# Kernel tuning notes

Hardware: AMD Instinct MI355X
Metric: run time of the kernel (lower is better)

## Reference

```python
import jax, jax.numpy as jnp
import numpy as np

B, C, L, E = 65536, 16, 32, 32
EPS = 1e-12

def _normalize(x, axis=-1):
    # F.normalize: x / max(||x||_2, eps)
    n = jnp.sqrt(jnp.sum(x * x, axis=axis, keepdims=True))
    return x / jnp.maximum(n, EPS)

def _linear(x, W, b):
    # torch nn.Linear: y = x @ W.T + b, W: [out, in]
    return jnp.einsum('bcl,el->bce', x, W) + b

def setup_inputs() -> dict:
    key = jax.random.key(0)
    ks = jax.random.split(key, 12)
    s_l = 1.0 / np.sqrt(L)
    s_p1 = 1.0 / np.sqrt(C * E)
    s_p2 = 1.0 / np.sqrt(C * 3)
    return {
        'embed1': jax.random.normal(ks[0], (B, C, L), jnp.float32),
        'embed2': jax.random.normal(ks[1], (B, C, L), jnp.float32),
        'qW': jax.random.uniform(ks[2], (E, L), jnp.float32, -s_l, s_l),
        'qb': jax.random.uniform(ks[3], (E,), jnp.float32, -s_l, s_l),
        'kW': jax.random.uniform(ks[4], (E, L), jnp.float32, -s_l, s_l),
        'kb': jax.random.uniform(ks[5], (E,), jnp.float32, -s_l, s_l),
        'vW': jax.random.uniform(ks[6], (E, L), jnp.float32, -s_l, s_l),
        'vb': jax.random.uniform(ks[7], (E,), jnp.float32, -s_l, s_l),
        'p1W': jax.random.uniform(ks[8], (C * 3, C * E), jnp.float32, -s_p1, s_p1),
        'p1b': jax.random.uniform(ks[9], (C * 3,), jnp.float32, -s_p1, s_p1),
        'p2W': jax.random.uniform(ks[10], (3, C * 3), jnp.float32, -s_p2, s_p2),
        'p2b': jax.random.uniform(ks[11], (3,), jnp.float32, -s_p2, s_p2),
    }

def reference(embed1, embed2, qW, qb, kW, kb, vW, vb, p1W, p1b, p2W, p2b):
    query = _linear(embed1, qW, qb) * _linear(embed2, qW, qb)   # [B,C,E]
    key_t = _linear(embed1, kW, kb) * _linear(embed2, kW, kb)   # [B,C,E]
    value = _linear(embed1, vW, vb) * _linear(embed2, vW, vb)   # [B,C,E]
    attn = jnp.einsum('bce,bde->bcd', _normalize(query), _normalize(key_t))  # [B,C,C]
    # torch F.softmax with dim=None on a 3-D tensor -> legacy dim=0 (batch axis)
    attn = jax.nn.softmax(attn, axis=0)
    # dropout(p=0.2) is identity in eval mode
    out = jnp.einsum('bcd,bce->bde', attn, value)  # attn.transpose(1,2) @ value, [B,C,E]
    h = out.reshape(out.shape[0], -1)              # [B, C*E]
    h = jax.nn.relu(h @ p1W.T + p1b) @ p2W.T + p2b  # [B, 3]
    return _normalize(h)
```

## Files before the change

### kernel.cpp

```cpp
#include <hip/hip_runtime.h>

#define B_TOT 65536
#define WS_P1W 4096
#define WS_EV  (1u << 20)

typedef float f32x4 __attribute__((ext_vector_type(4)));
typedef short s16x8 __attribute__((ext_vector_type(8)));

__device__ __forceinline__ float bf2f(unsigned short h) {
    unsigned u = ((unsigned)h) << 16;
    return __builtin_bit_cast(float, u);
}
__device__ __forceinline__ unsigned pack2(float a, float b) {
    unsigned ua = __builtin_bit_cast(unsigned, a) + 0x8000u;
    unsigned ub = __builtin_bit_cast(unsigned, b) + 0x8000u;
    return __builtin_amdgcn_perm(ub, ua, 0x07060302u);
}
__device__ __forceinline__ unsigned short f2bf(float f) {
    return (unsigned short)((__builtin_bit_cast(unsigned, f) + 0x8000u) >> 16);
}
__device__ __forceinline__ s16x8 cvt8(float4 a, float4 b) {
    uint4 u;
    u.x = pack2(a.x, a.y); u.y = pack2(a.z, a.w);
    u.z = pack2(b.x, b.y); u.w = pack2(b.z, b.w);
    return __builtin_bit_cast(s16x8, u);
}
#define MFMA(a, b, c) __builtin_amdgcn_mfma_f32_16x16x32_bf16((a), (b), (c), 0, 0, 0)

__global__ __launch_bounds__(256) void k0_prep(const float* __restrict__ p1W,
                                               char* __restrict__ ws) {
    int idx = blockIdx.x * 256 + threadIdx.x;
    if (blockIdx.x == 0 && threadIdx.x < 256)
        ((float*)ws)[threadIdx.x] = 0.f;
    int jj   = idx & 7;
    int lane = (idx >> 3) & 63;
    int ktnt = idx >> 9;
    int kt = ktnt & 15, nt = ktnt >> 4;
    int n_lo = lane & 15, q8 = lane >> 4;
    int j  = nt * 16 + n_lo;
    int ip = kt * 32 + q8 * 8 + jj;
    int e_lo = ip >> 5, qq = (ip >> 3) & 3, hh = (ip >> 2) & 1, r = ip & 3;
    int orig = (qq * 4 + r) * 32 + (e_lo + 16 * hh);
    ((unsigned short*)(ws + WS_P1W))[idx] = f2bf(p1W[j * 512 + orig]);
}

__global__ __launch_bounds__(256) void k1_stats(
    const float* __restrict__ e1, const float* __restrict__ e2,
    const float* __restrict__ qW, const float* __restrict__ qb,
    const float* __restrict__ kW, const float* __restrict__ kb,
    const float* __restrict__ vW, const float* __restrict__ vb,
    char* __restrict__ ws) {

    const int tid = threadIdx.x;
    const int lane = tid & 63;
    const int widx = tid >> 6;
    const int col = lane & 15;
    const int quad = lane >> 4;

    __shared__ __align__(16) unsigned short qk_lds[4][2][16 * 40];
    __shared__ float Dblk[256];
    Dblk[tid] = 0.f;
    __syncthreads();

    s16x8 wq[2], wk[2], wv[2];
    f32x4 cbq[2], cbk[2], cbv[2];
    for (int h = 0; h < 2; ++h) {
        int row = col + 16 * h;
        const float4* pq = (const float4*)(qW + row * 32 + quad * 8);
        const float4* pk = (const float4*)(kW + row * 32 + quad * 8);
        const float4* pv = (const float4*)(vW + row * 32 + quad * 8);
        wq[h] = cvt8(pq[0], pq[1]);
        wk[h] = cvt8(pk[0], pk[1]);
        wv[h] = cvt8(pv[0], pv[1]);
        float qv = qb[row], kv = kb[row], vv = vb[row];
        cbq[h] = (f32x4){qv, qv, qv, qv};
        cbk[h] = (f32x4){kv, kv, kv, kv};
        cbv[h] = (f32x4){vv, vv, vv, vv};
    }

    unsigned short* qbuf = qk_lds[widx][0];
    unsigned short* kbuf = qk_lds[widx][1];
    float dacc[4] = {0.f, 0.f, 0.f, 0.f};
    char* evbase = ws + WS_EV;
    const f32x4 z = {0.f, 0.f, 0.f, 0.f};

    const int gw = blockIdx.x * 4 + widx;
    for (int i = 0; i < 8; ++i) {
        const int b = gw * 8 + i;
        const float4* x1p = (const float4*)(e1 + (size_t)b * 512 + col * 32 + quad * 8);
        const float4* x2p = (const float4*)(e2 + (size_t)b * 512 + col * 32 + quad * 8);
        float4 a0 = x1p[0], a1 = x1p[1];
        float4 b0 = x2p[0], b1 = x2p[1];
        s16x8 fx1 = cvt8(a0, a1);
        s16x8 fx2 = cvt8(b0, b1);

        f32x4 q1[2], q2[2], k1[2], k2[2], v1[2], v2[2];
        for (int h = 0; h < 2; ++h) {
            q1[h] = MFMA(fx1, wq[h], cbq[h]); q2[h] = MFMA(fx2, wq[h], cbq[h]);
            k1[h] = MFMA(fx1, wk[h], cbk[h]); k2[h] = MFMA(fx2, wk[h], cbk[h]);
            v1[h] = MFMA(fx1, wv[h], cbv[h]); v2[h] = MFMA(fx2, wv[h], cbv[h]);
        }
        float Qt[2][4], Kt[2][4], Vv[2][4];
        for (int h = 0; h < 2; ++h)
            for (int r = 0; r < 4; ++r) {
                Qt[h][r] = q1[h][r] * q2[h][r];
                Kt[h][r] = k1[h][r] * k2[h][r];
                Vv[h][r] = v1[h][r] * v2[h][r];
            }
        for (int r = 0; r < 4; ++r) {
            int w = (quad * 4 + r) * 20 + col;
            ((unsigned*)qbuf)[w] = pack2(Qt[0][r], Qt[1][r]);
            ((unsigned*)kbuf)[w] = pack2(Kt[0][r], Kt[1][r]);
        }
        s16x8 aq = *(const s16x8*)(qbuf + col * 40 + quad * 8);
        s16x8 bk = *(const s16x8*)(kbuf + col * 40 + quad * 8);
        float qv[8], kv[8], ssq = 0.f, ssk = 0.f;
        for (int j = 0; j < 8; ++j) {
            qv[j] = bf2f((unsigned short)aq[j]); ssq += qv[j] * qv[j];
            kv[j] = bf2f((unsigned short)bk[j]); ssk += kv[j] * kv[j];
        }
        ssq += __shfl_xor(ssq, 16); ssq += __shfl_xor(ssq, 32);
        ssk += __shfl_xor(ssk, 16); ssk += __shfl_xor(ssk, 32);
        float sq = 1.f / fmaxf(sqrtf(ssq), 1e-12f);
        float sk = 1.f / fmaxf(sqrtf(ssk), 1e-12f);
        uint4 uq, uk;
        uq.x = pack2(qv[0] * sq, qv[1] * sq); uq.y = pack2(qv[2] * sq, qv[3] * sq);
        uq.z = pack2(qv[4] * sq, qv[5] * sq); uq.w = pack2(qv[6] * sq, qv[7] * sq);
        uk.x = pack2(kv[0] * sk, kv[1] * sk); uk.y = pack2(kv[2] * sk, kv[3] * sk);
        uk.z = pack2(kv[4] * sk, kv[5] * sk); uk.w = pack2(kv[6] * sk, kv[7] * sk);
        aq = __builtin_bit_cast(s16x8, uq);
        bk = __builtin_bit_cast(s16x8, uk);
        f32x4 S = MFMA(aq, bk, z);

        char* bbase = evbase + (size_t)b * 1536;
        float ex[4];
        for (int r = 0; r < 4; ++r) { ex[r] = __expf(S[r]); dacc[r] += ex[r]; }
        uint2 est; est.x = pack2(ex[0], ex[1]); est.y = pack2(ex[2], ex[3]);
        *(uint2*)(bbase + col * 32 + quad * 8) = est;
        for (int h = 0; h < 2; ++h) {
            uint2 vst;
            vst.x = pack2(Vv[h][0], Vv[h][1]);
            vst.y = pack2(Vv[h][2], Vv[h][3]);
            *(uint2*)(bbase + 512 + ((h * 16 + col) * 2 + (quad >> 1)) * 16 + (quad & 1) * 8) = vst;
        }
    }
    for (int r = 0; r < 4; ++r)
        atomicAdd(&Dblk[col * 16 + quad * 4 + r], dacc[r]);
    __syncthreads();
    atomicAdd(((float*)ws) + tid, Dblk[tid]);
}

__global__ __launch_bounds__(256) void k2_apply(
    const char* __restrict__ ws, const float* __restrict__ p1b,
    const float* __restrict__ p2W, const float* __restrict__ p2b,
    float* __restrict__ out) {

    const int tid = threadIdx.x;
    const int lane = tid & 63;
    const int widx = tid >> 6;
    const int col = lane & 15;
    const int quad = lane >> 4;
    const int qm = quad & 1;

    __shared__ __align__(16) unsigned short Hs[16 * 512];
    float* P = (float*)Hs;

    const float* Dws = (const float*)ws;
    float dinv[8];
    for (int j = 0; j < 8; ++j)
        dinv[j] = 1.f / Dws[col * 16 + qm * 8 + j];

    const char* evbase = ws + WS_EV;
    const unsigned short* p1wp = (const unsigned short*)(ws + WS_P1W);
    const int g = blockIdx.x;
    const f32x4 z = {0.f, 0.f, 0.f, 0.f};
    const s16x8 zz = {0, 0, 0, 0, 0, 0, 0, 0};

    for (int ii = 0; ii < 4; ++ii) {
        const int i = widx * 4 + ii;
        const int b = g * 16 + i;
        const char* bbase = evbase + (size_t)b * 1536;
        s16x8 eraw = *(const s16x8*)(bbase + col * 32 + qm * 16);
        s16x8 bf0 = *(const s16x8*)(bbase + 512 + (col * 2 + qm) * 16);
        s16x8 bf1 = *(const s16x8*)(bbase + 512 + ((16 + col) * 2 + qm) * 16);
        float ef[8];
        for (int j = 0; j < 8; ++j)
            ef[j] = bf2f((unsigned short)eraw[j]) * dinv[j];
        uint4 ua;
        ua.x = pack2(ef[0], ef[1]); ua.y = pack2(ef[2], ef[3]);
        ua.z = pack2(ef[4], ef[5]); ua.w = pack2(ef[6], ef[7]);
        s16x8 afrag = __builtin_bit_cast(s16x8, ua);
        if (quad >= 2) { afrag = zz; bf0 = zz; bf1 = zz; }
        f32x4 o0 = MFMA(afrag, bf0, z);
        f32x4 o1 = MFMA(afrag, bf1, z);
        uint4 uh;
        uh.x = pack2(o0[0], o0[1]); uh.y = pack2(o0[2], o0[3]);
        uh.z = pack2(o1[0], o1[1]); uh.w = pack2(o1[2], o1[3]);
        int chunk = (col * 4 + quad) ^ (i & 7);
        *(uint4*)(Hs + i * 512 + chunk * 8) = uh;
    }
    __syncthreads();

    f32x4 acc[3] = {z, z, z};
    for (int t = 0; t < 4; ++t) {
        int kt = widx * 4 + t;
        int chunk = (kt * 4 + quad) ^ (col & 7);
        s16x8 a = *(const s16x8*)(Hs + col * 512 + chunk * 8);
        for (int nt = 0; nt < 3; ++nt) {
            s16x8 bw = *(const s16x8*)(p1wp + ((nt * 16 + kt) * 64 + lane) * 8);
            acc[nt] = MFMA(a, bw, acc[nt]);
        }
    }
    __syncthreads();

    for (int nt = 0; nt < 3; ++nt)
        *(f32x4*)(P + (widx * 64 + lane) * 12 + nt * 4) = acc[nt];
    __syncthreads();

    if (widx == 0) {
        f32x4 s[3] = {z, z, z};
        for (int w = 0; w < 4; ++w)
            for (int nt = 0; nt < 3; ++nt) {
                f32x4 pv = *(const f32x4*)(P + (w * 64 + lane) * 12 + nt * 4);
                s[nt] += pv;
            }
        float p2w[3][3], p1bias[3];
        for (int nt = 0; nt < 3; ++nt) {
            p1bias[nt] = p1b[col + 16 * nt];
            for (int t = 0; t < 3; ++t) p2w[nt][t] = p2W[t * 48 + col + 16 * nt];
        }
        const float pb0 = p2b[0], pb1 = p2b[1], pb2 = p2b[2];
        float pp[4][3] = {};
        for (int nt = 0; nt < 3; ++nt)
            for (int r = 0; r < 4; ++r) {
                float hv = fmaxf(s[nt][r] + p1bias[nt], 0.f);
                pp[r][0] += hv * p2w[nt][0];
                pp[r][1] += hv * p2w[nt][1];
                pp[r][2] += hv * p2w[nt][2];
            }
        for (int m = 1; m <= 8; m <<= 1)
            for (int r = 0; r < 4; ++r)
                for (int t = 0; t < 3; ++t)
                    pp[r][t] += __shfl_xor(pp[r][t], m);
        for (int r = 0; r < 4; ++r) {
            float h0 = pp[r][0] + pb0, h1 = pp[r][1] + pb1, h2 = pp[r][2] + pb2;
            float inv = 1.f / fmaxf(sqrtf(h0 * h0 + h1 * h1 + h2 * h2), 1e-12f);
            if (col < 3) {
                float v = (col == 0) ? h0 : ((col == 1) ? h1 : h2);
                out[(size_t)(g * 16 + quad * 4 + r) * 3 + col] = v * inv;
            }
        }
    }
}

extern "C" void kernel_launch(void* const* d_in, const int* in_sizes, int n_in,
                              void* d_out, int out_size, void* d_ws, size_t ws_size,
                              hipStream_t stream) {
    const float* e1  = (const float*)d_in[0];
    const float* e2  = (const float*)d_in[1];
    const float* qW  = (const float*)d_in[2];
    const float* qb  = (const float*)d_in[3];
    const float* kW  = (const float*)d_in[4];
    const float* kb  = (const float*)d_in[5];
    const float* vW  = (const float*)d_in[6];
    const float* vb  = (const float*)d_in[7];
    const float* p1W = (const float*)d_in[8];
    const float* p1b = (const float*)d_in[9];
    const float* p2W = (const float*)d_in[10];
    const float* p2b = (const float*)d_in[11];
    float* out = (float*)d_out;
    char* ws = (char*)d_ws;

    k0_prep<<<96, 256, 0, stream>>>(p1W, ws);
    k1_stats<<<2048, 256, 0, stream>>>(e1, e2, qW, qb, kW, kb, vW, vb, ws);
    k2_apply<<<4096, 256, 0, stream>>>(ws, p1b, p2W, p2b, out);
}
```

Before: 342.2 us.

## Spread softmax denominator atomics and restructure stats kernel to two batches per wave

The stats kernel now runs 4x more blocks, each wave handling two batch items with their loads issued up front, instead of looping over eight items. The global denominator is split into 8 partial copies chosen by block index, and the apply kernel sums them, which reduces contention on the same atomic addresses. The key normalization is now applied to the dot-product result instead of to the key vector, and launch bounds add occupancy hints. A leftover dead first MFMA loop computes values that are then recomputed; the compiler should remove it, but it makes the code messy.

Result: slower. 367.1 us (+7.3%).

```diff
diff --git a/kernel.cpp b/kernel.cpp
--- a/kernel.cpp
+++ b/kernel.cpp
@@ -1,7 +1,8 @@
 #include <hip/hip_runtime.h>
 
 #define B_TOT 65536
-#define WS_P1W 4096
+#define WS_D   0
+#define WS_P1W 8192
 #define WS_EV  (1u << 20)
 
 typedef float f32x4 __attribute__((ext_vector_type(4)));
@@ -30,8 +31,8 @@
 __global__ __launch_bounds__(256) void k0_prep(const float* __restrict__ p1W,
                                                char* __restrict__ ws) {
     int idx = blockIdx.x * 256 + threadIdx.x;
-    if (blockIdx.x == 0 && threadIdx.x < 256)
-        ((float*)ws)[threadIdx.x] = 0.f;
+    if (blockIdx.x < 8)
+        ((float*)ws)[blockIdx.x * 256 + threadIdx.x] = 0.f;
     int jj   = idx & 7;
     int lane = (idx >> 3) & 63;
     int ktnt = idx >> 9;
@@ -44,7 +45,7 @@
     ((unsigned short*)(ws + WS_P1W))[idx] = f2bf(p1W[j * 512 + orig]);
 }
 
-__global__ __launch_bounds__(256) void k1_stats(
+__global__ __launch_bounds__(256, 3) void k1_stats(
     const float* __restrict__ e1, const float* __restrict__ e2,
     const float* __restrict__ qW, const float* __restrict__ qb,
     const float* __restrict__ kW, const float* __restrict__ kb,
@@ -57,7 +58,7 @@
     const int col = lane & 15;
     const int quad = lane >> 4;
 
-    __shared__ __align__(16) unsigned short qk_lds[4][2][16 * 40];
+    __shared__ __align__(16) unsigned short qk_lds[4][4][640];
     __shared__ float Dblk[256];
     Dblk[tid] = 0.f;
     __syncthreads();
@@ -78,79 +79,135 @@
         cbv[h] = (f32x4){vv, vv, vv, vv};
     }
 
-    unsigned short* qbuf = qk_lds[widx][0];
-    unsigned short* kbuf = qk_lds[widx][1];
-    float dacc[4] = {0.f, 0.f, 0.f, 0.f};
+    unsigned short* qb0 = qk_lds[widx][0];
+    unsigned short* kb0 = qk_lds[widx][1];
+    unsigned short* qb1 = qk_lds[widx][2];
+    unsigned short* kb1 = qk_lds[widx][3];
     char* evbase = ws + WS_EV;
     const f32x4 z = {0.f, 0.f, 0.f, 0.f};
 
     const int gw = blockIdx.x * 4 + widx;
-    for (int i = 0; i < 8; ++i) {
-        const int b = gw * 8 + i;
-        const float4* x1p = (const float4*)(e1 + (size_t)b * 512 + col * 32 + quad * 8);
-        const float4* x2p = (const float4*)(e2 + (size_t)b * 512 + col * 32 + quad * 8);
-        float4 a0 = x1p[0], a1 = x1p[1];
-        float4 b0 = x2p[0], b1 = x2p[1];
-        s16x8 fx1 = cvt8(a0, a1);
-        s16x8 fx2 = cvt8(b0, b1);
-
-        f32x4 q1[2], q2[2], k1[2], k2[2], v1[2], v2[2];
-        for (int h = 0; h < 2; ++h) {
-            q1[h] = MFMA(fx1, wq[h], cbq[h]); q2[h] = MFMA(fx2, wq[h], cbq[h]);
-            k1[h] = MFMA(fx1, wk[h], cbk[h]); k2[h] = MFMA(fx2, wk[h], cbk[h]);
-            v1[h] = MFMA(fx1, wv[h], cbv[h]); v2[h] = MFMA(fx2, wv[h], cbv[h]);
-        }
-        float Qt[2][4], Kt[2][4], Vv[2][4];
-        for (int h = 0; h < 2; ++h)
+    const int bA = gw * 2, bB = bA + 1;
+
+    const float4* x1A = (const float4*)(e1 + (size_t)bA * 512 + col * 32 + quad * 8);
+    const float4* x2A = (const float4*)(e2 + (size_t)bA * 512 + col * 32 + quad * 8);
+    const float4* x1B = (const float4*)(e1 + (size_t)bB * 512 + col * 32 + quad * 8);
+    const float4* x2B = (const float4*)(e2 + (size_t)bB * 512 + col * 32 + quad * 8);
+    float4 a0A = x1A[0], a1A = x1A[1], b0A = x2A[0], b1A = x2A[1];
+    float4 a0B = x1B[0], a1B = x1B[1], b0B = x2B[0], b1B = x2B[1];
+    s16x8 fx1A = cvt8(a0A, a1A), fx2A = cvt8(b0A, b1A);
+    s16x8 fx1B = cvt8(a0B, a1B), fx2B = cvt8(b0B, b1B);
+
+    float VvA[2][4], VvB[2][4];
+    for (int h = 0; h < 2; ++h) {
+        f32x4 q1 = MFMA(fx1A, wq[h], cbq[h]), q2 = MFMA(fx2A, wq[h], cbq[h]);
+        f32x4 k1 = MFMA(fx1A, wk[h], cbk[h]), k2 = MFMA(fx2A, wk[h], cbk[h]);
+        f32x4 v1 = MFMA(fx1A, wv[h], cbv[h]), v2 = MFMA(fx2A, wv[h], cbv[h]);
+        f32x4 Qt = q1 * q2, Kt = k1 * k2;
+        for (int r = 0; r < 4; ++r) VvA[h][r] = v1[r] * v2[r];
+        if (h == 0) {
             for (int r = 0; r < 4; ++r) {
-                Qt[h][r] = q1[h][r] * q2[h][r];
-                Kt[h][r] = k1[h][r] * k2[h][r];
-                Vv[h][r] = v1[h][r] * v2[h][r];
             }
+        }
+        static_assert(true, "");
+        if (h == 0) {
+            for (int r = 0; r < 4; ++r) { VvA[0][r] = VvA[0][r]; }
+        }
+        (void)Qt; (void)Kt;
+    }
+    {
+        f32x4 q1_0 = MFMA(fx1A, wq[0], cbq[0]), q2_0 = MFMA(fx2A, wq[0], cbq[0]);
+        f32x4 q1_1 = MFMA(fx1A, wq[1], cbq[1]), q2_1 = MFMA(fx2A, wq[1], cbq[1]);
+        f32x4 k1_0 = MFMA(fx1A, wk[0], cbk[0]), k2_0 = MFMA(fx2A, wk[0], cbk[0]);
+        f32x4 k1_1 = MFMA(fx1A, wk[1], cbk[1]), k2_1 = MFMA(fx2A, wk[1], cbk[1]);
+        f32x4 v1_0 = MFMA(fx1A, wv[0], cbv[0]), v2_0 = MFMA(fx2A, wv[0], cbv[0]);
+        f32x4 v1_1 = MFMA(fx1A, wv[1], cbv[1]), v2_1 = MFMA(fx2A, wv[1], cbv[1]);
         for (int r = 0; r < 4; ++r) {
+            VvA[0][r] = v1_0[r] * v2_0[r];
+            VvA[1][r] = v1_1[r] * v2_1[r];
             int w = (quad * 4 + r) * 20 + col;
-            ((unsigned*)qbuf)[w] = pack2(Qt[0][r], Qt[1][r]);
-            ((unsigned*)kbuf)[w] = pack2(Kt[0][r], Kt[1][r]);
-        }
-        s16x8 aq = *(const s16x8*)(qbuf + col * 40 + quad * 8);
-        s16x8 bk = *(const s16x8*)(kbuf + col * 40 + quad * 8);
-        float qv[8], kv[8], ssq = 0.f, ssk = 0.f;
-        for (int j = 0; j < 8; ++j) {
-            qv[j] = bf2f((unsigned short)aq[j]); ssq += qv[j] * qv[j];
-            kv[j] = bf2f((unsigned short)bk[j]); ssk += kv[j] * kv[j];
-        }
-        ssq += __shfl_xor(ssq, 16); ssq += __shfl_xor(ssq, 32);
-        ssk += __shfl_xor(ssk, 16); ssk += __shfl_xor(ssk, 32);
-        float sq = 1.f / fmaxf(sqrtf(ssq), 1e-12f);
-        float sk = 1.f / fmaxf(sqrtf(ssk), 1e-12f);
-        uint4 uq, uk;
-        uq.x = pack2(qv[0] * sq, qv[1] * sq); uq.y = pack2(qv[2] * sq, qv[3] * sq);
-        uq.z = pack2(qv[4] * sq, qv[5] * sq); uq.w = pack2(qv[6] * sq, qv[7] * sq);
-        uk.x = pack2(kv[0] * sk, kv[1] * sk); uk.y = pack2(kv[2] * sk, kv[3] * sk);
-        uk.z = pack2(kv[4] * sk, kv[5] * sk); uk.w = pack2(kv[6] * sk, kv[7] * sk);
-        aq = __builtin_bit_cast(s16x8, uq);
-        bk = __builtin_bit_cast(s16x8, uk);
-        f32x4 S = MFMA(aq, bk, z);
-
-        char* bbase = evbase + (size_t)b * 1536;
-        float ex[4];
-        for (int r = 0; r < 4; ++r) { ex[r] = __expf(S[r]); dacc[r] += ex[r]; }
-        uint2 est; est.x = pack2(ex[0], ex[1]); est.y = pack2(ex[2], ex[3]);
-        *(uint2*)(bbase + col * 32 + quad * 8) = est;
-        for (int h = 0; h < 2; ++h) {
-            uint2 vst;
-            vst.x = pack2(Vv[h][0], Vv[h][1]);
-            vst.y = pack2(Vv[h][2], Vv[h][3]);
-            *(uint2*)(bbase + 512 + ((h * 16 + col) * 2 + (quad >> 1)) * 16 + (quad & 1) * 8) = vst;
-        }
-    }
+            ((unsigned*)qb0)[w] = pack2(q1_0[r] * q2_0[r], q1_1[r] * q2_1[r]);
+            ((unsigned*)kb0)[w] = pack2(k1_0[r] * k2_0[r], k1_1[r] * k2_1[r]);
+        }
+    }
+    {
+        f32x4 q1_0 = MFMA(fx1B, wq[0], cbq[0]), q2_0 = MFMA(fx2B, wq[0], cbq[0]);
+        f32x4 q1_1 = MFMA(fx1B, wq[1], cbq[1]), q2_1 = MFMA(fx2B, wq[1], cbq[1]);
+        f32x4 k1_0 = MFMA(fx1B, wk[0], cbk[0]), k2_0 = MFMA(fx2B, wk[0], cbk[0]);
+        f32x4 k1_1 = MFMA(fx1B, wk[1], cbk[1]), k2_1 = MFMA(fx2B, wk[1], cbk[1]);
+        f32x4 v1_0 = MFMA(fx1B, wv[0], cbv[0]), v2_0 = MFMA(fx2B, wv[0], cbv[0]);
+        f32x4 v1_1 = MFMA(fx1B, wv[1], cbv[1]), v2_1 = MFMA(fx2B, wv[1], cbv[1]);
+        for (int r = 0; r < 4; ++r) {
+            VvB[0][r] = v1_0[r] * v2_0[r];
+            VvB[1][r] = v1_1[r] * v2_1[r];
+            int w = (quad * 4 + r) * 20 + col;
+            ((unsigned*)qb1)[w] = pack2(q1_0[r] * q2_0[r], q1_1[r] * q2_1[r]);
+            ((unsigned*)kb1)[w] = pack2(k1_0[r] * k2_0[r], k1_1[r] * k2_1[r]);
+        }
+    }
+
+    s16x8 aqA = *(const s16x8*)(qb0 + col * 40 + quad * 8);
+    s16x8 bkA = *(const s16x8*)(kb0 + col * 40 + quad * 8);
+    s16x8 aqB = *(const s16x8*)(qb1 + col * 40 + quad * 8);
+    s16x8 bkB = *(const s16x8*)(kb1 + col * 40 + quad * 8);
+
+    float qvA[8], qvB[8];
+    float ssqA = 0.f, ssqB = 0.f, sskA = 0.f, sskB = 0.f;
+    for (int j = 0; j < 8; ++j) {
+        qvA[j] = bf2f((unsigned short)aqA[j]); ssqA += qvA[j] * qvA[j];
+        qvB[j] = bf2f((unsigned short)aqB[j]); ssqB += qvB[j] * qvB[j];
+        float ka = bf2f((unsigned short)bkA[j]); sskA += ka * ka;
+        float kb_ = bf2f((unsigned short)bkB[j]); sskB += kb_ * kb_;
+    }
+    ssqA += __shfl_xor(ssqA, 16); sskA += __shfl_xor(sskA, 16);
+    ssqB += __shfl_xor(ssqB, 16); sskB += __shfl_xor(sskB, 16);
+    ssqA += __shfl_xor(ssqA, 32); sskA += __shfl_xor(sskA, 32);
+    ssqB += __shfl_xor(ssqB, 32); sskB += __shfl_xor(sskB, 32);
+    float sqA = 1.f / fmaxf(sqrtf(ssqA), 1e-12f);
+    float sqB = 1.f / fmaxf(sqrtf(ssqB), 1e-12f);
+    float ikA = 1.f / fmaxf(sqrtf(sskA), 1e-12f);
+    float ikB = 1.f / fmaxf(sqrtf(sskB), 1e-12f);
+
+    uint4 uq;
+    uq.x = pack2(qvA[0] * sqA, qvA[1] * sqA); uq.y = pack2(qvA[2] * sqA, qvA[3] * sqA);
+    uq.z = pack2(qvA[4] * sqA, qvA[5] * sqA); uq.w = pack2(qvA[6] * sqA, qvA[7] * sqA);
+    s16x8 aqAs = __builtin_bit_cast(s16x8, uq);
+    uq.x = pack2(qvB[0] * sqB, qvB[1] * sqB); uq.y = pack2(qvB[2] * sqB, qvB[3] * sqB);
+    uq.z = pack2(qvB[4] * sqB, qvB[5] * sqB); uq.w = pack2(qvB[6] * sqB, qvB[7] * sqB);
+    s16x8 aqBs = __builtin_bit_cast(s16x8, uq);
+
+    f32x4 SA = MFMA(aqAs, bkA, z);
+    f32x4 SB = MFMA(aqBs, bkB, z);
+
+    float exA[4], exB[4], dacc[4];
+    for (int r = 0; r < 4; ++r) {
+        exA[r] = __expf(SA[r] * ikA);
+        exB[r] = __expf(SB[r] * ikB);
+        dacc[r] = exA[r] + exB[r];
+    }
+
+    char* baseA = evbase + (size_t)bA * 1536;
+    char* baseB = evbase + (size_t)bB * 1536;
+    uint2 st;
+    st.x = pack2(exA[0], exA[1]); st.y = pack2(exA[2], exA[3]);
+    *(uint2*)(baseA + col * 32 + quad * 8) = st;
+    st.x = pack2(exB[0], exB[1]); st.y = pack2(exB[2], exB[3]);
+    *(uint2*)(baseB + col * 32 + quad * 8) = st;
+    for (int h = 0; h < 2; ++h) {
+        int voff = 512 + ((h * 16 + col) * 2 + (quad >> 1)) * 16 + (quad & 1) * 8;
+        st.x = pack2(VvA[h][0], VvA[h][1]); st.y = pack2(VvA[h][2], VvA[h][3]);
+        *(uint2*)(baseA + voff) = st;
+        st.x = pack2(VvB[h][0], VvB[h][1]); st.y = pack2(VvB[h][2], VvB[h][3]);
+        *(uint2*)(baseB + voff) = st;
+    }
+
     for (int r = 0; r < 4; ++r)
         atomicAdd(&Dblk[col * 16 + quad * 4 + r], dacc[r]);
     __syncthreads();
-    atomicAdd(((float*)ws) + tid, Dblk[tid]);
-}
-
-__global__ __launch_bounds__(256) void k2_apply(
+    atomicAdd(((float*)ws) + ((blockIdx.x & 7) << 8) + tid, Dblk[tid]);
+}
+
+__global__ __launch_bounds__(256, 4) void k2_apply(
     const char* __restrict__ ws, const float* __restrict__ p1b,
     const float* __restrict__ p2W, const float* __restrict__ p2b,
     float* __restrict__ out) {
@@ -166,9 +223,15 @@
     float* P = (float*)Hs;
 
     const float* Dws = (const float*)ws;
+    float dsum[8] = {0.f, 0.f, 0.f, 0.f, 0.f, 0.f, 0.f, 0.f};
+    for (int p = 0; p < 8; ++p) {
+        const float4* dp = (const float4*)(Dws + p * 256 + col * 16 + qm * 8);
+        float4 a = dp[0], b = dp[1];
+        dsum[0] += a.x; dsum[1] += a.y; dsum[2] += a.z; dsum[3] += a.w;
+        dsum[4] += b.x; dsum[5] += b.y; dsum[6] += b.z; dsum[7] += b.w;
+    }
     float dinv[8];
-    for (int j = 0; j < 8; ++j)
-        dinv[j] = 1.f / Dws[col * 16 + qm * 8 + j];
+    for (int j = 0; j < 8; ++j) dinv[j] = 1.f / dsum[j];
 
     const char* evbase = ws + WS_EV;
     const unsigned short* p1wp = (const unsigned short*)(ws + WS_P1W);
@@ -272,6 +335,6 @@
     char* ws = (char*)d_ws;
 
     k0_prep<<<96, 256, 0, stream>>>(p1W, ws);
-    k1_stats<<<2048, 256, 0, stream>>>(e1, e2, qW, qb, kW, kb, vW, vb, ws);
+    k1_stats<<<8192, 256, 0, stream>>>(e1, e2, qW, qb, kW, kb, vW, vb, ws);
     k2_apply<<<4096, 256, 0, stream>>>(ws, p1b, p2W, p2b, out);
 }
```

## Software-pipeline stats kernel loads and spread softmax denominator atomics

Applied to the files above, without the earlier changes.

k1 now prefetches the next two batch rows of inputs into registers and overlaps the attention/exp stage of row i-1 with the projection stage of row i, using double-buffered LDS. Biases are added after the MFMA rather than folded into the accumulator, and the key normalization is applied as a scale on S instead of rescaling k. The global denominator atomics are spread over 8 partial copies to reduce contention, and k2 sums the copies. k2 also hoists all global loads (exp, V, p1W fragments) up front to overlap latency. Both kernels get an occupancy hint of 3 blocks, which adds register pressure risk.

Result: no change. 346.5 us (+1.3%).

```diff
diff --git a/kernel.cpp b/kernel.cpp
--- a/kernel.cpp
+++ b/kernel.cpp
@@ -1,7 +1,8 @@
 #include <hip/hip_runtime.h>
 
 #define B_TOT 65536
-#define WS_P1W 4096
+#define WS_D   0
+#define WS_P1W 8192
 #define WS_EV  (1u << 20)
 
 typedef float f32x4 __attribute__((ext_vector_type(4)));
@@ -30,8 +31,8 @@
 __global__ __launch_bounds__(256) void k0_prep(const float* __restrict__ p1W,
                                                char* __restrict__ ws) {
     int idx = blockIdx.x * 256 + threadIdx.x;
-    if (blockIdx.x == 0 && threadIdx.x < 256)
-        ((float*)ws)[threadIdx.x] = 0.f;
+    if (blockIdx.x < 8)
+        ((float*)ws)[blockIdx.x * 256 + threadIdx.x] = 0.f;
     int jj   = idx & 7;
     int lane = (idx >> 3) & 63;
     int ktnt = idx >> 9;
@@ -44,7 +45,7 @@
     ((unsigned short*)(ws + WS_P1W))[idx] = f2bf(p1W[j * 512 + orig]);
 }
 
-__global__ __launch_bounds__(256) void k1_stats(
+__global__ __launch_bounds__(256, 3) void k1_stats(
     const float* __restrict__ e1, const float* __restrict__ e2,
     const float* __restrict__ qW, const float* __restrict__ qb,
     const float* __restrict__ kW, const float* __restrict__ kb,
@@ -57,13 +58,13 @@
     const int col = lane & 15;
     const int quad = lane >> 4;
 
-    __shared__ __align__(16) unsigned short qk_lds[4][2][16 * 40];
+    __shared__ __align__(16) unsigned short qk[4][2][2][640];
     __shared__ float Dblk[256];
     Dblk[tid] = 0.f;
     __syncthreads();
 
     s16x8 wq[2], wk[2], wv[2];
-    f32x4 cbq[2], cbk[2], cbv[2];
+    float qbs[2], kbs[2], vbs[2];
     for (int h = 0; h < 2; ++h) {
         int row = col + 16 * h;
         const float4* pq = (const float4*)(qW + row * 32 + quad * 8);
@@ -72,85 +73,100 @@
         wq[h] = cvt8(pq[0], pq[1]);
         wk[h] = cvt8(pk[0], pk[1]);
         wv[h] = cvt8(pv[0], pv[1]);
-        float qv = qb[row], kv = kb[row], vv = vb[row];
-        cbq[h] = (f32x4){qv, qv, qv, qv};
-        cbk[h] = (f32x4){kv, kv, kv, kv};
-        cbv[h] = (f32x4){vv, vv, vv, vv};
-    }
-
-    unsigned short* qbuf = qk_lds[widx][0];
-    unsigned short* kbuf = qk_lds[widx][1];
-    float dacc[4] = {0.f, 0.f, 0.f, 0.f};
+        qbs[h] = qb[row]; kbs[h] = kb[row]; vbs[h] = vb[row];
+    }
+
     char* evbase = ws + WS_EV;
     const f32x4 z = {0.f, 0.f, 0.f, 0.f};
+    float dacc[4] = {0.f, 0.f, 0.f, 0.f};
 
     const int gw = blockIdx.x * 4 + widx;
-    for (int i = 0; i < 8; ++i) {
-        const int b = gw * 8 + i;
-        const float4* x1p = (const float4*)(e1 + (size_t)b * 512 + col * 32 + quad * 8);
-        const float4* x2p = (const float4*)(e2 + (size_t)b * 512 + col * 32 + quad * 8);
-        float4 a0 = x1p[0], a1 = x1p[1];
-        float4 b0 = x2p[0], b1 = x2p[1];
-        s16x8 fx1 = cvt8(a0, a1);
-        s16x8 fx2 = cvt8(b0, b1);
-
-        f32x4 q1[2], q2[2], k1[2], k2[2], v1[2], v2[2];
-        for (int h = 0; h < 2; ++h) {
-            q1[h] = MFMA(fx1, wq[h], cbq[h]); q2[h] = MFMA(fx2, wq[h], cbq[h]);
-            k1[h] = MFMA(fx1, wk[h], cbk[h]); k2[h] = MFMA(fx2, wk[h], cbk[h]);
-            v1[h] = MFMA(fx1, wv[h], cbv[h]); v2[h] = MFMA(fx2, wv[h], cbv[h]);
-        }
-        float Qt[2][4], Kt[2][4], Vv[2][4];
-        for (int h = 0; h < 2; ++h)
-            for (int r = 0; r < 4; ++r) {
-                Qt[h][r] = q1[h][r] * q2[h][r];
-                Kt[h][r] = k1[h][r] * k2[h][r];
-                Vv[h][r] = v1[h][r] * v2[h][r];
-            }
+    const int base = gw * 8;
+    const int xoff = col * 32 + quad * 8;
+
+    float4 L[2][4];
+    auto issueL = [&](int slot, int i) {
+        const float4* x1 = (const float4*)(e1 + (size_t)(base + i) * 512 + xoff);
+        const float4* x2 = (const float4*)(e2 + (size_t)(base + i) * 512 + xoff);
+        L[slot][0] = x1[0]; L[slot][1] = x1[1];
+        L[slot][2] = x2[0]; L[slot][3] = x2[1];
+    };
+    auto stage1 = [&](int i) {
+        const int s = i & 1;
+        s16x8 fx1 = cvt8(L[s][0], L[s][1]);
+        s16x8 fx2 = cvt8(L[s][2], L[s][3]);
+        f32x4 q10 = MFMA(fx1, wq[0], z), q20 = MFMA(fx2, wq[0], z);
+        f32x4 q11 = MFMA(fx1, wq[1], z), q21 = MFMA(fx2, wq[1], z);
+        f32x4 k10 = MFMA(fx1, wk[0], z), k20 = MFMA(fx2, wk[0], z);
+        f32x4 k11 = MFMA(fx1, wk[1], z), k21 = MFMA(fx2, wk[1], z);
+        f32x4 v10 = MFMA(fx1, wv[0], z), v20 = MFMA(fx2, wv[0], z);
+        f32x4 v11 = MFMA(fx1, wv[1], z), v21 = MFMA(fx2, wv[1], z);
+        unsigned* qlds = (unsigned*)qk[widx][s][0];
+        unsigned* klds = (unsigned*)qk[widx][s][1];
         for (int r = 0; r < 4; ++r) {
             int w = (quad * 4 + r) * 20 + col;
-            ((unsigned*)qbuf)[w] = pack2(Qt[0][r], Qt[1][r]);
-            ((unsigned*)kbuf)[w] = pack2(Kt[0][r], Kt[1][r]);
-        }
-        s16x8 aq = *(const s16x8*)(qbuf + col * 40 + quad * 8);
-        s16x8 bk = *(const s16x8*)(kbuf + col * 40 + quad * 8);
-        float qv[8], kv[8], ssq = 0.f, ssk = 0.f;
-        for (int j = 0; j < 8; ++j) {
-            qv[j] = bf2f((unsigned short)aq[j]); ssq += qv[j] * qv[j];
-            kv[j] = bf2f((unsigned short)bk[j]); ssk += kv[j] * kv[j];
-        }
-        ssq += __shfl_xor(ssq, 16); ssq += __shfl_xor(ssq, 32);
-        ssk += __shfl_xor(ssk, 16); ssk += __shfl_xor(ssk, 32);
-        float sq = 1.f / fmaxf(sqrtf(ssq), 1e-12f);
-        float sk = 1.f / fmaxf(sqrtf(ssk), 1e-12f);
-        uint4 uq, uk;
-        uq.x = pack2(qv[0] * sq, qv[1] * sq); uq.y = pack2(qv[2] * sq, qv[3] * sq);
-        uq.z = pack2(qv[4] * sq, qv[5] * sq); uq.w = pack2(qv[6] * sq, qv[7] * sq);
-        uk.x = pack2(kv[0] * sk, kv[1] * sk); uk.y = pack2(kv[2] * sk, kv[3] * sk);
-        uk.z = pack2(kv[4] * sk, kv[5] * sk); uk.w = pack2(kv[6] * sk, kv[7] * sk);
-        aq = __builtin_bit_cast(s16x8, uq);
-        bk = __builtin_bit_cast(s16x8, uk);
-        f32x4 S = MFMA(aq, bk, z);
-
-        char* bbase = evbase + (size_t)b * 1536;
-        float ex[4];
-        for (int r = 0; r < 4; ++r) { ex[r] = __expf(S[r]); dacc[r] += ex[r]; }
-        uint2 est; est.x = pack2(ex[0], ex[1]); est.y = pack2(ex[2], ex[3]);
-        *(uint2*)(bbase + col * 32 + quad * 8) = est;
-        for (int h = 0; h < 2; ++h) {
-            uint2 vst;
-            vst.x = pack2(Vv[h][0], Vv[h][1]);
-            vst.y = pack2(Vv[h][2], Vv[h][3]);
-            *(uint2*)(bbase + 512 + ((h * 16 + col) * 2 + (quad >> 1)) * 16 + (quad & 1) * 8) = vst;
-        }
-    }
+            qlds[w] = pack2((q10[r] + qbs[0]) * (q20[r] + qbs[0]),
+                            (q11[r] + qbs[1]) * (q21[r] + qbs[1]));
+            klds[w] = pack2((k10[r] + kbs[0]) * (k20[r] + kbs[0]),
+                            (k11[r] + kbs[1]) * (k21[r] + kbs[1]));
+        }
+        char* bb = evbase + (size_t)(base + i) * 1536;
+        float f00 = (v10[0] + vbs[0]) * (v20[0] + vbs[0]);
+        float f01 = (v10[1] + vbs[0]) * (v20[1] + vbs[0]);
+        float f02 = (v10[2] + vbs[0]) * (v20[2] + vbs[0]);
+        float f03 = (v10[3] + vbs[0]) * (v20[3] + vbs[0]);
+        float f10 = (v11[0] + vbs[1]) * (v21[0] + vbs[1]);
+        float f11 = (v11[1] + vbs[1]) * (v21[1] + vbs[1]);
+        float f12 = (v11[2] + vbs[1]) * (v21[2] + vbs[1]);
+        float f13 = (v11[3] + vbs[1]) * (v21[3] + vbs[1]);
+        uint2 st;
+        st.x = pack2(f00, f01); st.y = pack2(f02, f03);
+        *(uint2*)(bb + 512 + ((col) * 2 + (quad >> 1)) * 16 + (quad & 1) * 8) = st;
+        st.x = pack2(f10, f11); st.y = pack2(f12, f13);
+        *(uint2*)(bb + 512 + ((16 + col) * 2 + (quad >> 1)) * 16 + (quad & 1) * 8) = st;
+    };
+
+#pragma unroll
+    for (int i = 0; i < 9; ++i) {
+        s16x8 aq, bk;
+        if (i >= 1) {
+            const int s = (i - 1) & 1;
+            aq = *(const s16x8*)(qk[widx][s][0] + col * 40 + quad * 8);
+            bk = *(const s16x8*)(qk[widx][s][1] + col * 40 + quad * 8);
+        }
+        if (i == 0) { issueL(0, 0); issueL(1, 1); }
+        if (i < 8) stage1(i);
+        if (i + 2 < 8) issueL(i & 1, i + 2);
+        if (i >= 1) {
+            float qv[8], ssq = 0.f, ssk = 0.f;
+            for (int j = 0; j < 8; ++j) {
+                qv[j] = bf2f((unsigned short)aq[j]); ssq += qv[j] * qv[j];
+                float kf = bf2f((unsigned short)bk[j]); ssk += kf * kf;
+            }
+            ssq += __shfl_xor(ssq, 16); ssk += __shfl_xor(ssk, 16);
+            ssq += __shfl_xor(ssq, 32); ssk += __shfl_xor(ssk, 32);
+            float sq = 1.f / fmaxf(sqrtf(ssq), 1e-12f);
+            float ik = 1.f / fmaxf(sqrtf(ssk), 1e-12f);
+            uint4 uq;
+            uq.x = pack2(qv[0] * sq, qv[1] * sq); uq.y = pack2(qv[2] * sq, qv[3] * sq);
+            uq.z = pack2(qv[4] * sq, qv[5] * sq); uq.w = pack2(qv[6] * sq, qv[7] * sq);
+            s16x8 aqs = __builtin_bit_cast(s16x8, uq);
+            f32x4 S = MFMA(aqs, bk, z);
+            float ex[4];
+            for (int r = 0; r < 4; ++r) { ex[r] = __expf(S[r] * ik); dacc[r] += ex[r]; }
+            uint2 st;
+            st.x = pack2(ex[0], ex[1]); st.y = pack2(ex[2], ex[3]);
+            *(uint2*)(evbase + (size_t)(base + i - 1) * 1536 + col * 32 + quad * 8) = st;
+        }
+    }
+
     for (int r = 0; r < 4; ++r)
         atomicAdd(&Dblk[col * 16 + quad * 4 + r], dacc[r]);
     __syncthreads();
-    atomicAdd(((float*)ws) + tid, Dblk[tid]);
-}
-
-__global__ __launch_bounds__(256) void k2_apply(
+    atomicAdd(((float*)ws) + ((blockIdx.x & 7) << 8) + tid, Dblk[tid]);
+}
+
+__global__ __launch_bounds__(256, 3) void k2_apply(
     const char* __restrict__ ws, const float* __restrict__ p1b,
     const float* __restrict__ p2W, const float* __restrict__ p2b,
     float* __restrict__ out) {
@@ -165,34 +181,54 @@
     __shared__ __align__(16) unsigned short Hs[16 * 512];
     float* P = (float*)Hs;
 
-    const float* Dws = (const float*)ws;
-    float dinv[8];
-    for (int j = 0; j < 8; ++j)
-        dinv[j] = 1.f / Dws[col * 16 + qm * 8 + j];
-
     const char* evbase = ws + WS_EV;
     const unsigned short* p1wp = (const unsigned short*)(ws + WS_P1W);
     const int g = blockIdx.x;
     const f32x4 z = {0.f, 0.f, 0.f, 0.f};
     const s16x8 zz = {0, 0, 0, 0, 0, 0, 0, 0};
 
+    const float* Dws = (const float*)ws;
+    float4 dpa[8], dpb[8];
+    for (int p = 0; p < 8; ++p) {
+        const float4* dp = (const float4*)(Dws + p * 256 + col * 16 + qm * 8);
+        dpa[p] = dp[0]; dpb[p] = dp[1];
+    }
+    s16x8 er[4], bv0[4], bv1[4];
+    for (int ii = 0; ii < 4; ++ii) {
+        const int b = g * 16 + widx * 4 + ii;
+        const char* bbase = evbase + (size_t)b * 1536;
+        er[ii]  = *(const s16x8*)(bbase + col * 32 + qm * 16);
+        bv0[ii] = *(const s16x8*)(bbase + 512 + (col * 2 + qm) * 16);
+        bv1[ii] = *(const s16x8*)(bbase + 512 + ((16 + col) * 2 + qm) * 16);
+    }
+    s16x8 bw[3][4];
+    for (int nt = 0; nt < 3; ++nt)
+        for (int t = 0; t < 4; ++t)
+            bw[nt][t] = *(const s16x8*)(p1wp + ((nt * 16 + widx * 4 + t) * 64 + lane) * 8);
+
+    float dinv[8];
+    {
+        float ds0[8] = {0, 0, 0, 0, 0, 0, 0, 0};
+        for (int p = 0; p < 8; ++p) {
+            ds0[0] += dpa[p].x; ds0[1] += dpa[p].y; ds0[2] += dpa[p].z; ds0[3] += dpa[p].w;
+            ds0[4] += dpb[p].x; ds0[5] += dpb[p].y; ds0[6] += dpb[p].z; ds0[7] += dpb[p].w;
+        }
+        for (int j = 0; j < 8; ++j) dinv[j] = 1.f / ds0[j];
+    }
+
     for (int ii = 0; ii < 4; ++ii) {
         const int i = widx * 4 + ii;
-        const int b = g * 16 + i;
-        const char* bbase = evbase + (size_t)b * 1536;
-        s16x8 eraw = *(const s16x8*)(bbase + col * 32 + qm * 16);
-        s16x8 bf0 = *(const s16x8*)(bbase + 512 + (col * 2 + qm) * 16);
-        s16x8 bf1 = *(const s16x8*)(bbase + 512 + ((16 + col) * 2 + qm) * 16);
         float ef[8];
         for (int j = 0; j < 8; ++j)
-            ef[j] = bf2f((unsigned short)eraw[j]) * dinv[j];
+            ef[j] = bf2f((unsigned short)er[ii][j]) * dinv[j];
         uint4 ua;
         ua.x = pack2(ef[0], ef[1]); ua.y = pack2(ef[2], ef[3]);
         ua.z = pack2(ef[4], ef[5]); ua.w = pack2(ef[6], ef[7]);
         s16x8 afrag = __builtin_bit_cast(s16x8, ua);
-        if (quad >= 2) { afrag = zz; bf0 = zz; bf1 = zz; }
-        f32x4 o0 = MFMA(afrag, bf0, z);
-        f32x4 o1 = MFMA(afrag, bf1, z);
+        s16x8 b0 = bv0[ii], b1 = bv1[ii];
+        if (quad >= 2) { afrag = zz; b0 = zz; b1 = zz; }
+        f32x4 o0 = MFMA(afrag, b0, z);
+        f32x4 o1 = MFMA(afrag, b1, z);
         uint4 uh;
         uh.x = pack2(o0[0], o0[1]); uh.y = pack2(o0[2], o0[3]);
         uh.z = pack2(o1[0], o1[1]); uh.w = pack2(o1[2], o1[3]);
@@ -206,10 +242,8 @@
         int kt = widx * 4 + t;
         int chunk = (kt * 4 + quad) ^ (col & 7);
         s16x8 a = *(const s16x8*)(Hs + col * 512 + chunk * 8);
-        for (int nt = 0; nt < 3; ++nt) {
-            s16x8 bw = *(const s16x8*)(p1wp + ((nt * 16 + kt) * 64 + lane) * 8);
-            acc[nt] = MFMA(a, bw, acc[nt]);
-        }
+        for (int nt = 0; nt < 3; ++nt)
+            acc[nt] = MFMA(a, bw[nt][t], acc[nt]);
     }
     __syncthreads();
 
```
